# Performance work log

Hardware: AMD Instinct MI355X
Metric: run time of the kernel (lower is better)

## Reference

```python
import jax, jax.numpy as jnp
import numpy as np

NUM_LEVELS = 4
RADIUS = 4
H, W = 64, 128


def _bilinear_sample(feat, x, y):
    # feat: [N, Hl, Wl]; x, y: [N, K, K] pixel coords; zeros padding, align_corners=True
    N, Hl, Wl = feat.shape
    x0 = jnp.floor(x)
    y0 = jnp.floor(y)
    x1 = x0 + 1.0
    y1 = y0 + 1.0
    wx1 = x - x0
    wx0 = 1.0 - wx1
    wy1 = y - y0
    wy0 = 1.0 - wy1
    n_idx = jnp.arange(N)[:, None, None]

    def gather(xi, yi):
        inb = (xi >= 0) & (xi <= Wl - 1) & (yi >= 0) & (yi <= Hl - 1)
        xc = jnp.clip(xi, 0, Wl - 1).astype(jnp.int32)
        yc = jnp.clip(yi, 0, Hl - 1).astype(jnp.int32)
        v = feat[n_idx, yc, xc]
        return jnp.where(inb, v, jnp.zeros((), feat.dtype))

    return (gather(x0, y0) * wx0 * wy0 + gather(x1, y0) * wx1 * wy0
            + gather(x0, y1) * wx0 * wy1 + gather(x1, y1) * wx1 * wy1)


def _correlation(fmap1, fmap2, coords):
    bs, dim, h, w = fmap1.shape
    f1 = fmap1.reshape(bs, dim, h * w)
    f2 = fmap2.reshape(bs, dim, h * w)
    cv = jnp.einsum('bdm,bdn->bmn', f1, f2) / jnp.sqrt(jnp.asarray(dim, jnp.float32))
    cv = cv.reshape(bs * h * w, h, w)
    pyramid = [cv]
    for _ in range(NUM_LEVELS - 1):
        N, hl, wl = cv.shape
        cv = cv.reshape(N, hl // 2, 2, wl // 2, 2).mean(axis=(2, 4))  # avg_pool2d(2,2)
        pyramid.append(cv)

    cxy = coords.transpose(0, 2, 3, 1).astype(jnp.float32)  # [bs,h,w,2]
    cx = cxy[..., 0].reshape(-1)  # [bs*h*w]
    cy = cxy[..., 1].reshape(-1)
    r = RADIUS
    d = jnp.linspace(-r, r, 2 * r + 1, dtype=jnp.float32)
    dy, dx = jnp.meshgrid(d, d, indexing='ij')  # [K,K]

    outs = []
    for i, corr in enumerate(pyramid):
        scale = jnp.float32(2 ** i)
        x = cx[:, None, None] / scale + dx[None]
        y = cy[:, None, None] / scale + dy[None]
        sampled = _bilinear_sample(corr, x, y)  # [bs*h*w, K, K]
        outs.append(sampled.reshape(bs, h, w, -1))
    out = jnp.concatenate(outs, axis=-1)  # [bs,h,w,num_levels*K*K]
    return out.transpose(0, 3, 1, 2)


def setup_inputs() -> dict:
    key = jax.random.key(0)
    k1, k2, k3, k4 = jax.random.split(key, 4)
    fmap1 = jax.random.normal(k1, (1, 256, H, W), dtype=jnp.float32)
    fmap2 = jax.random.normal(k2, (1, 256, H, W), dtype=jnp.float32)
    cx = jax.random.uniform(k3, (1, 1, H, W), dtype=jnp.float32) * (W - 1)
    cy = jax.random.uniform(k4, (1, 1, H, W), dtype=jnp.float32) * (H - 1)
    coords = jnp.concatenate([cx, cy], axis=1)  # [1,2,H,W], channel 0 = x, 1 = y
    return {"fmap1": fmap1, "fmap2": fmap2, "coords": coords}


def reference(fmap1, fmap2, coords):
    return _correlation(fmap1, fmap2, coords)
```

## Files before the change

kernel.cpp:

```cpp
#include <hip/hip_runtime.h>
#include <stdint.h>

typedef _Float16 f16;
typedef __attribute__((ext_vector_type(8))) _Float16 f16x8;
typedef __attribute__((ext_vector_type(4))) float f32x4;
typedef __attribute__((ext_vector_type(2))) float fv2;
typedef __attribute__((ext_vector_type(4))) float fv4;

#define H0 64
#define W0 128
#define NPIX 8192
#define KD 256
#define NCAT 10880
#define OFF1 8192
#define OFF2 10240
#define OFF3 10752
#define CAP0 640
#define CAP1 2048
#define PL1OFF (32 * CAP0)
#define PLTOT (PL1OFF + 8 * CAP1)
#define ZTOT (64 + PLTOT + 64)


__global__ __launch_bounds__(256) void fused_pre(const float* __restrict__ in0,
                                                 const float* __restrict__ in1,
                                                 f16* __restrict__ At,
                                                 f16* __restrict__ Bt,
                                                 int* __restrict__ cnt) {
  __shared__ f16 tile[64][65];
  int bid = blockIdx.x;
  int t = threadIdx.x;

  if (bid < 1024) {
    const float* in = (bid < 512) ? in0 : in1;
    f16* out = (bid < 512) ? At : Bt;
    size_t NR = (bid < 512) ? NPIX : NCAT;
    int bx = bid & 511;
    int m0 = (bx & 127) * 64;
    int d0 = (bx >> 7) * 64;
    int a = t & 63, b = t >> 6;
#pragma unroll
    for (int i = 0; i < 16; ++i) {
      int d = b + i * 4;
      tile[a][d] = (f16)in[(size_t)(d0 + d) * NPIX + m0 + a];
    }
    __syncthreads();
#pragma unroll
    for (int i = 0; i < 16; ++i) {
      int m = b + i * 4;
      int d = d0 + a;
      out[((size_t)(d >> 5) * NR + (m0 + m)) * 32 + (d & 31)] = tile[m][a];
    }
  } else if (bid < 1360) {
    int idx = (bid - 1024) * 256 + t;
    float acc[8] = {0, 0, 0, 0, 0, 0, 0, 0};
    int r, dc;
    if (idx < 65536) {
      int r1 = idx & 2047; dc = idx >> 11; r = r1;
      int y = r1 >> 6, x = r1 & 63;
#pragma unroll
      for (int e = 0; e < 8; ++e) {
        const float* p = in1 + (size_t)(dc * 8 + e) * NPIX + (y * 2) * W0 + x * 2;
        fv2 s0 = *(const fv2*)p;
        fv2 s1 = *(const fv2*)(p + W0);
        acc[e] = (s0[0] + s0[1] + s1[0] + s1[1]) * 0.25f;
      }
    } else if (idx < 81920) {
      int i2 = idx - 65536;
      int r2 = i2 & 511; dc = i2 >> 9; r = 2048 + r2;
      int y = r2 >> 5, x = r2 & 31;
#pragma unroll
      for (int e = 0; e < 8; ++e) {
        const float* p = in1 + (size_t)(dc * 8 + e) * NPIX + (y * 4) * W0 + x * 4;
        float s = 0.f;
#pragma unroll
        for (int h = 0; h < 4; ++h) {
          fv4 v = *(const fv4*)(p + h * W0);
          s += v[0] + v[1] + v[2] + v[3];
        }
        acc[e] = s * 0.0625f;
      }
    } else {
      int i3 = idx - 81920;
      int r3 = i3 & 127; dc = i3 >> 7; r = 2560 + r3;
      int y = r3 >> 4, x = r3 & 15;
#pragma unroll
      for (int e = 0; e < 8; ++e) {
        const float* p = in1 + (size_t)(dc * 8 + e) * NPIX + (y * 8) * W0 + x * 8;
        float s = 0.f;
#pragma unroll
        for (int h = 0; h < 8; ++h) {
          fv4 v0 = *(const fv4*)(p + h * W0);
          fv4 v1 = *(const fv4*)(p + h * W0 + 4);
          s += v0[0] + v0[1] + v0[2] + v0[3] + v1[0] + v1[1] + v1[2] + v1[3];
        }
        acc[e] = s * 0.015625f;
      }
    }
    f16x8 o;
#pragma unroll
    for (int e = 0; e < 8; ++e) o[e] = (f16)acc[e];
    *(f16x8*)(Bt + ((size_t)(dc >> 2) * NCAT + 8192 + r) * 32 + (dc & 3) * 8) = o;
  } else {
    int idx = (bid - 1360) * 256 + t;
    if (idx < ZTOT) cnt[idx] = 0;
  }
}

__global__ __launch_bounds__(1024) void bucket_build(const float* __restrict__ coords,
                                                     int2* __restrict__ meta,
                                                     int* __restrict__ cnt) {
  __shared__ int hist[40];
  __shared__ int base[40];
  int* plist = cnt + 64;
  int t = threadIdx.x;
  int m = blockIdx.x * 1024 + t;
  if (t < 40) hist[t] = 0;
  __syncthreads();

  float cx = coords[m];
  float cy = coords[NPIX + m];
  int X0l[2], Y0l[2];
  int mx = 0, my = 0;
#pragma unroll
  for (int lev = 0; lev < 4; ++lev) {
    float inv = 1.0f / (float)(1 << lev);
    int X0 = (int)floorf(cx * inv) - 4;
    int Y0 = (int)floorf(cy * inv) - 4;
    if (lev < 2) { X0l[lev] = X0; Y0l[lev] = Y0; }
    mx |= (X0 & 0xff) << (8 * lev);
    my |= (Y0 & 0xff) << (8 * lev);
  }
  meta[m] = make_int2(mx, my);

  int b0 = (min(max(Y0l[0], 0), 63) >> 4) * 8 + (min(max(X0l[0], 0), 127) >> 4);
  int b1 = (min(max(Y0l[1], 0), 31) >> 4) * 4 + (min(max(X0l[1], 0), 63) >> 4);
  int s0 = atomicAdd(&hist[b0], 1);
  int s1 = atomicAdd(&hist[32 + b1], 1);
  __syncthreads();

  if (t < 40) base[t] = atomicAdd(&cnt[t], hist[t]);
  __syncthreads();

  int p0 = base[b0] + s0;
  if (p0 < CAP0) plist[b0 * CAP0 + p0] = m;
  int p1 = base[32 + b1] + s1;
  if (p1 < CAP1) plist[PL1OFF + b1 * CAP1 + p1] = m;
}

__global__ __launch_bounds__(256, 2) void gemm_all(const f16* __restrict__ At,
                                                   const f16* __restrict__ Bt,
                                                   const int* __restrict__ cnt,
                                                   const int2* __restrict__ meta,
                                                   f16* __restrict__ Wbuf) {
  __shared__ f16 sa[8192];
  const int* plist = cnt + 64;
  int bid = blockIdx.x;
  int t = threadIdx.x;
  int lane = t & 63;
  int w = t >> 6;
  int lr = lane & 15;
  int ko = lane >> 4;

  if (bid < 160) {
    int bm = (((bid & 7) << 2) | ((bid >> 3) & 3)) << 8;
    int bn = OFF2 + ((bid >> 5) << 7);

    const f16* Ab = At + (size_t)(bm + w * 64 + lr) * 32 + ko * 8;
    const f16* Bb = Bt + (size_t)(bn + lr) * 32 + ko * 8;

    f16x8 af[2][4], bf[2][8];
#define LOADK(s, kk)                                                           \
    do {                                                                       \
      const f16* ap = Ab + (size_t)(kk) * (NPIX * 32);                         \
      const f16* bp = Bb + (size_t)(kk) * (NCAT * 32);                         \
      _Pragma("unroll")                                                        \
      for (int i = 0; i < 4; ++i) af[s][i] = *(const f16x8*)(ap + i * 512);    \
      _Pragma("unroll")                                                        \
      for (int i = 0; i < 8; ++i) bf[s][i] = *(const f16x8*)(bp + i * 512);    \
    } while (0)

    f32x4 acc[4][8];
#pragma unroll
    for (int i = 0; i < 4; ++i)
#pragma unroll
      for (int j = 0; j < 8; ++j) acc[i][j] = (f32x4){0.f, 0.f, 0.f, 0.f};

    LOADK(0, 0);
    LOADK(1, 1);
#pragma unroll
    for (int kk = 0; kk < 8; ++kk) {
      const int cur = kk & 1;
#pragma unroll
      for (int mi = 0; mi < 4; ++mi)
#pragma unroll
        for (int ni = 0; ni < 8; ++ni)
          acc[mi][ni] = __builtin_amdgcn_mfma_f32_16x16x32_f16(
              af[cur][mi], bf[cur][ni], acc[mi][ni], 0, 0, 0);
      if (kk + 2 < 8) LOADK(cur, kk + 2);
    }
#undef LOADK

    int lev, n0, wlog;
    if (bn < OFF3) { lev = 2; n0 = bn - OFF2; wlog = 5; }
    else           { lev = 3; n0 = bn - OFF3; wlog = 4; }
    int wmask = (1 << wlog) - 1;
    int yA = n0 >> wlog;
    int yB = (n0 + 127) >> wlog;
    int ycol[8], xcol[8];
#pragma unroll
    for (int ni = 0; ni < 8; ++ni) {
      int n = n0 + ni * 16 + lr;
      ycol[ni] = n >> wlog;
      xcol[ni] = n & wmask;
    }
    int sh = lev * 8;
#pragma unroll
    for (int mi = 0; mi < 4; ++mi)
#pragma unroll
      for (int r2 = 0; r2 < 4; ++r2) {
        int grow = bm + w * 64 + mi * 16 + ko * 4 + r2;
        int2 mv = meta[grow];
        int Y0 = (int)(signed char)((mv.y >> sh) & 0xff);
        if (Y0 <= yB && Y0 + 9 >= yA) {
          int X0 = (int)(signed char)((mv.x >> sh) & 0xff);
          f16* rowp = Wbuf + (size_t)grow * 512 + lev * 128;
#pragma unroll
          for (int ni = 0; ni < 8; ++ni) {
            int dy = ycol[ni] - Y0;
            int dx = xcol[ni] - X0;
            if ((unsigned)dy < 10u && (unsigned)dx < 10u)
              rowp[dy * 12 + dx] = (f16)(acc[mi][ni][r2] * 0.0625f);
          }
        }
      }
    return;
  }

  int bb = bid - 160;
  int lev, b, mg, half;
  if (bb < 1280) { lev = 0; b = bb / 40; int r = bb % 40; mg = r >> 1; half = r & 1; }
  else { lev = 1; int i = bb - 1280; b = i / 128; int r = i % 128; mg = r >> 1; half = r & 1; }

  int CAP   = lev ? CAP1 : CAP0;
  int cb    = min(cnt[lev ? 32 + b : b], CAP);
  if (mg * 32 >= cb) return;
  int Hl    = lev ? 32 : 64;
  int Wmap  = lev ? 64 : 128;
  int bx    = lev ? (b & 3) : (b & 7);
  int by    = lev ? (b >> 2) : (b >> 3);
  int x0 = bx * 16, y0 = by * 16;
  int NY = min(25, Hl - y0);
  int rowbase = lev ? 8192 : 0;
  int pbase = (lev ? PL1OFF + b * CAP1 : b * CAP0) + mg * 32;

  {
    int spix = t >> 3;
    int skk  = t & 7;
    int sp = plist[pbase + spix] & (NPIX - 1);
    const f16* g = At + (size_t)skk * (NPIX * 32) + (size_t)sp * 32;
    int line = spix >> 1;
    int sb = (spix & 1) * 4;
    f16* dst = sa + skk * 1024 + line * 64;
#pragma unroll
    for (int q = 0; q < 4; ++q) {
      int phys = (sb + q) ^ (line & 7);
      *(f16x8*)(dst + phys * 8) = *(const f16x8*)(g + q * 8);
    }
  }

  int aoff[2];
#pragma unroll
  for (int mi = 0; mi < 2; ++mi) {
    int pl = mi * 16 + lr;
    int line = pl >> 1;
    int phys = ((pl & 1) * 4 + ko) ^ (line & 7);
    aoff[mi] = line * 64 + phys * 8;
  }

  bool vst[4];
  int brow[4];
#pragma unroll
  for (int st = 0; st < 4; ++st) {
    int q = w + 4 * st;
    int yl = half * 13 + q;
    vst[st] = (q < (half ? 12 : 13)) && (yl < NY);
    int ylc = min(yl, NY - 1);
    brow[st] = rowbase + (y0 + ylc) * Wmap + x0 + lr;
  }

  f16x8 bf[2][8];
#define BLDB(s_, kk_)                                                          \
  do {                                                                         \
    const f16* bp = Bt + (size_t)(kk_) * (NCAT * 32) + ko * 8;                 \
    _Pragma("unroll")                                                          \
    for (int st = 0; st < 4; ++st) {                                           \
      bf[s_][st * 2]     = *(const f16x8*)(bp + (size_t)brow[st] * 32);        \
      bf[s_][st * 2 + 1] = *(const f16x8*)(bp + (size_t)(brow[st] + 16) * 32); \
    }                                                                          \
  } while (0)

  BLDB(0, 0);
  BLDB(1, 1);

  f32x4 acc[8][2];
#pragma unroll
  for (int i = 0; i < 8; ++i)
#pragma unroll
    for (int j = 0; j < 2; ++j) acc[i][j] = (f32x4){0.f, 0.f, 0.f, 0.f};

  __syncthreads();

#pragma unroll
  for (int kk = 0; kk < 8; ++kk) {
    const int cur = kk & 1;
    f16x8 a0 = *(const f16x8*)(sa + kk * 1024 + aoff[0]);
    f16x8 a1 = *(const f16x8*)(sa + kk * 1024 + aoff[1]);
#pragma unroll
    for (int nf = 0; nf < 8; ++nf) {
      acc[nf][0] = __builtin_amdgcn_mfma_f32_16x16x32_f16(a0, bf[cur][nf],
                                                          acc[nf][0], 0, 0, 0);
      acc[nf][1] = __builtin_amdgcn_mfma_f32_16x16x32_f16(a1, bf[cur][nf],
                                                          acc[nf][1], 0, 0, 0);
    }
    if (kk + 2 < 8) BLDB(cur, kk + 2);
  }
#undef BLDB

  int pe[2][4];
  int Xp[2][4], Yp[2][4];
  int sh = lev * 8;
#pragma unroll
  for (int mi = 0; mi < 2; ++mi)
#pragma unroll
    for (int r2 = 0; r2 < 4; ++r2) {
      int slot = mg * 32 + mi * 16 + ko * 4 + r2;
      int p = plist[pbase + mi * 16 + ko * 4 + r2] & (NPIX - 1);
      pe[mi][r2] = (slot < cb) ? p : -1;
      int2 mv = meta[p];
      Xp[mi][r2] = (int)(signed char)((mv.x >> sh) & 0xff);
      Yp[mi][r2] = (int)(signed char)((mv.y >> sh) & 0xff);
    }
#pragma unroll
  for (int st = 0; st < 4; ++st) {
    if (!vst[st]) continue;
    int y = y0 + half * 13 + w + 4 * st;
#pragma unroll
    for (int xc = 0; xc < 2; ++xc) {
      int x = x0 + xc * 16 + lr;
#pragma unroll
      for (int mi = 0; mi < 2; ++mi)
#pragma unroll
        for (int r2 = 0; r2 < 4; ++r2) {
          int p = pe[mi][r2];
          int dy = y - Yp[mi][r2];
          int dx = x - Xp[mi][r2];
          if (p >= 0 && (unsigned)dy < 10u && (unsigned)dx < 10u)
            Wbuf[(size_t)p * 512 + lev * 128 + dy * 12 + dx] =
                (f16)(acc[st * 2 + xc][mi][r2] * 0.0625f);
        }
    }
  }
}

__global__ __launch_bounds__(64) void corr_sample(const f16* __restrict__ Wbuf,
                                                  const float* __restrict__ coords,
                                                  float* __restrict__ out) {
  int tid = blockIdx.x * 64 + threadIdx.x;
  int m = tid & (NPIX - 1);
  int lev = tid >> 13;
  int Hl = H0 >> lev, Wl = W0 >> lev;

  float cx = coords[m];
  float cy = coords[NPIX + m];
  float inv = 1.0f / (float)(1 << lev);
  float xb = cx * inv, yb = cy * inv;
  float fx = floorf(xb), fy = floorf(yb);
  int X0 = (int)fx - 4, Y0 = (int)fy - 4;
  float wx1 = xb - fx, wx0 = 1.0f - wx1;
  float wy1 = yb - fy, wy0 = 1.0f - wy1;

  const f16* wb = Wbuf + (size_t)m * 512 + lev * 128;
  f16x8 rv[15];
#pragma unroll
  for (int i = 0; i < 15; ++i) rv[i] = *(const f16x8*)(wb + i * 8);

  float* op = out + (size_t)lev * 81 * NPIX + m;
  float cur[11], nxt[11];
#pragma unroll
  for (int i = 0; i < 11; ++i) {
    bool in = ((unsigned)Y0 < (unsigned)Hl) && ((unsigned)(X0 + i) < (unsigned)Wl);
    cur[i] = in ? (float)rv[i >> 3][i & 7] : 0.0f;
  }
#pragma unroll
  for (int j = 0; j < 9; ++j) {
    bool yin = (unsigned)(Y0 + j + 1) < (unsigned)Hl;
#pragma unroll
    for (int i = 0; i < 11; ++i) {
      int c = (j + 1) * 12 + i;
      bool in = yin && ((unsigned)(X0 + i) < (unsigned)Wl);
      nxt[i] = in ? (float)rv[c >> 3][c & 7] : 0.0f;
    }
#pragma unroll
    for (int i = 0; i < 9; ++i) {
      float v = wy0 * (wx0 * cur[i] + wx1 * cur[i + 1])
              + wy1 * (wx0 * nxt[i] + wx1 * nxt[i + 1]);
      op[(size_t)(j * 9 + i) * NPIX] = v;
    }
#pragma unroll
    for (int i = 0; i < 11; ++i) cur[i] = nxt[i];
  }
}

extern "C" void kernel_launch(void* const* d_in, const int* in_sizes, int n_in,
                              void* d_out, int out_size, void* d_ws, size_t ws_size,
                              hipStream_t stream) {
  const float* fmap1  = (const float*)d_in[0];
  const float* fmap2  = (const float*)d_in[1];
  const float* coords = (const float*)d_in[2];
  float* out = (float*)d_out;

  char* ws = (char*)d_ws;
  size_t offA = 0;
  size_t offB = offA + (size_t)NPIX * KD * 2;
  size_t offW = offB + (size_t)NCAT * KD * 2;
  size_t offM = offW + (size_t)NPIX * 512 * 2;
  size_t offC = offM + (size_t)NPIX * 8;
  size_t need = offC + (size_t)ZTOT * 4;
  if (ws_size < need) return;

  f16*  At   = (f16*)(ws + offA);
  f16*  Bt   = (f16*)(ws + offB);
  f16*  Wbuf = (f16*)(ws + offW);
  int2* meta = (int2*)(ws + offM);
  int*  cnt  = (int*)(ws + offC);

  fused_pre<<<1505, 256, 0, stream>>>(fmap1, fmap2, At, Bt, cnt);
  bucket_build<<<8, 1024, 0, stream>>>(coords, meta, cnt);
  gemm_all<<<2464, 256, 0, stream>>>(At, Bt, cnt, meta, Wbuf);
  corr_sample<<<512, 64, 0, stream>>>(Wbuf, coords, out);
}
```

Measured before the change: 73.35 us.

## Split dense and bucketed GEMM into separate kernels with XCD-aware block mapping

Splits the combined GEMM kernel into a dense kernel for the coarse pyramid levels and a bucketed kernel for the fine levels, so the bucketed kernel can use a higher occupancy launch bound. Bucketed blocks are remapped so that blocks sharing a bucket land on the same XCD, which should improve L2 reuse of B rows. The LDS swizzle of the A tile now also mixes in the k-slice index to reduce bank conflicts. The cost is an extra kernel launch, and the dense and bucketed GEMM work no longer run concurrently.

```diff
diff --git a/kernel.cpp b/kernel.cpp
--- a/kernel.cpp
+++ b/kernel.cpp
@@ -148,99 +148,103 @@
   if (p1 < CAP1) plist[PL1OFF + b1 * CAP1 + p1] = m;
 }
 
-__global__ __launch_bounds__(256, 2) void gemm_all(const f16* __restrict__ At,
-                                                   const f16* __restrict__ Bt,
-                                                   const int* __restrict__ cnt,
-                                                   const int2* __restrict__ meta,
-                                                   f16* __restrict__ Wbuf) {
-  __shared__ f16 sa[8192];
-  const int* plist = cnt + 64;
+__global__ __launch_bounds__(256, 2) void gemm_dense(const f16* __restrict__ At,
+                                                     const f16* __restrict__ Bt,
+                                                     const int2* __restrict__ meta,
+                                                     f16* __restrict__ Wbuf) {
   int bid = blockIdx.x;
+  int bm = (((bid & 7) << 2) | ((bid >> 3) & 3)) << 8;
+  int bn = OFF2 + ((bid >> 5) << 7);
+
   int t = threadIdx.x;
   int lane = t & 63;
   int w = t >> 6;
   int lr = lane & 15;
   int ko = lane >> 4;
 
-  if (bid < 160) {
-    int bm = (((bid & 7) << 2) | ((bid >> 3) & 3)) << 8;
-    int bn = OFF2 + ((bid >> 5) << 7);
-
-    const f16* Ab = At + (size_t)(bm + w * 64 + lr) * 32 + ko * 8;
-    const f16* Bb = Bt + (size_t)(bn + lr) * 32 + ko * 8;
-
-    f16x8 af[2][4], bf[2][8];
+  const f16* Ab = At + (size_t)(bm + w * 64 + lr) * 32 + ko * 8;
+  const f16* Bb = Bt + (size_t)(bn + lr) * 32 + ko * 8;
+
+  f16x8 af[2][4], bf[2][8];
 #define LOADK(s, kk)                                                           \
-    do {                                                                       \
-      const f16* ap = Ab + (size_t)(kk) * (NPIX * 32);                         \
-      const f16* bp = Bb + (size_t)(kk) * (NCAT * 32);                         \
-      _Pragma("unroll")                                                        \
-      for (int i = 0; i < 4; ++i) af[s][i] = *(const f16x8*)(ap + i * 512);    \
-      _Pragma("unroll")                                                        \
-      for (int i = 0; i < 8; ++i) bf[s][i] = *(const f16x8*)(bp + i * 512);    \
-    } while (0)
-
-    f32x4 acc[4][8];
-#pragma unroll
-    for (int i = 0; i < 4; ++i)
-#pragma unroll
-      for (int j = 0; j < 8; ++j) acc[i][j] = (f32x4){0.f, 0.f, 0.f, 0.f};
-
-    LOADK(0, 0);
-    LOADK(1, 1);
-#pragma unroll
-    for (int kk = 0; kk < 8; ++kk) {
-      const int cur = kk & 1;
-#pragma unroll
-      for (int mi = 0; mi < 4; ++mi)
-#pragma unroll
-        for (int ni = 0; ni < 8; ++ni)
-          acc[mi][ni] = __builtin_amdgcn_mfma_f32_16x16x32_f16(
-              af[cur][mi], bf[cur][ni], acc[mi][ni], 0, 0, 0);
-      if (kk + 2 < 8) LOADK(cur, kk + 2);
-    }
+  do {                                                                         \
+    const f16* ap = Ab + (size_t)(kk) * (NPIX * 32);                           \
+    const f16* bp = Bb + (size_t)(kk) * (NCAT * 32);                           \
+    _Pragma("unroll")                                                          \
+    for (int i = 0; i < 4; ++i) af[s][i] = *(const f16x8*)(ap + i * 512);      \
+    _Pragma("unroll")                                                          \
+    for (int i = 0; i < 8; ++i) bf[s][i] = *(const f16x8*)(bp + i * 512);      \
+  } while (0)
+
+  f32x4 acc[4][8];
+#pragma unroll
+  for (int i = 0; i < 4; ++i)
+#pragma unroll
+    for (int j = 0; j < 8; ++j) acc[i][j] = (f32x4){0.f, 0.f, 0.f, 0.f};
+
+  LOADK(0, 0);
+  LOADK(1, 1);
+#pragma unroll
+  for (int kk = 0; kk < 8; ++kk) {
+    const int cur = kk & 1;
+#pragma unroll
+    for (int mi = 0; mi < 4; ++mi)
+#pragma unroll
+      for (int ni = 0; ni < 8; ++ni)
+        acc[mi][ni] = __builtin_amdgcn_mfma_f32_16x16x32_f16(
+            af[cur][mi], bf[cur][ni], acc[mi][ni], 0, 0, 0);
+    if (kk + 2 < 8) LOADK(cur, kk + 2);
+  }
 #undef LOADK
 
-    int lev, n0, wlog;
-    if (bn < OFF3) { lev = 2; n0 = bn - OFF2; wlog = 5; }
-    else           { lev = 3; n0 = bn - OFF3; wlog = 4; }
-    int wmask = (1 << wlog) - 1;
-    int yA = n0 >> wlog;
-    int yB = (n0 + 127) >> wlog;
-    int ycol[8], xcol[8];
-#pragma unroll
-    for (int ni = 0; ni < 8; ++ni) {
-      int n = n0 + ni * 16 + lr;
-      ycol[ni] = n >> wlog;
-      xcol[ni] = n & wmask;
-    }
-    int sh = lev * 8;
-#pragma unroll
-    for (int mi = 0; mi < 4; ++mi)
-#pragma unroll
-      for (int r2 = 0; r2 < 4; ++r2) {
-        int grow = bm + w * 64 + mi * 16 + ko * 4 + r2;
-        int2 mv = meta[grow];
-        int Y0 = (int)(signed char)((mv.y >> sh) & 0xff);
-        if (Y0 <= yB && Y0 + 9 >= yA) {
-          int X0 = (int)(signed char)((mv.x >> sh) & 0xff);
-          f16* rowp = Wbuf + (size_t)grow * 512 + lev * 128;
-#pragma unroll
-          for (int ni = 0; ni < 8; ++ni) {
-            int dy = ycol[ni] - Y0;
-            int dx = xcol[ni] - X0;
-            if ((unsigned)dy < 10u && (unsigned)dx < 10u)
-              rowp[dy * 12 + dx] = (f16)(acc[mi][ni][r2] * 0.0625f);
-          }
+  int lev, n0, wlog;
+  if (bn < OFF3) { lev = 2; n0 = bn - OFF2; wlog = 5; }
+  else           { lev = 3; n0 = bn - OFF3; wlog = 4; }
+  int wmask = (1 << wlog) - 1;
+  int yA = n0 >> wlog;
+  int yB = (n0 + 127) >> wlog;
+  int ycol[8], xcol[8];
+#pragma unroll
+  for (int ni = 0; ni < 8; ++ni) {
+    int n = n0 + ni * 16 + lr;
+    ycol[ni] = n >> wlog;
+    xcol[ni] = n & wmask;
+  }
+  int sh = lev * 8;
+#pragma unroll
+  for (int mi = 0; mi < 4; ++mi)
+#pragma unroll
+    for (int r2 = 0; r2 < 4; ++r2) {
+      int grow = bm + w * 64 + mi * 16 + ko * 4 + r2;
+      int2 mv = meta[grow];
+      int Y0 = (int)(signed char)((mv.y >> sh) & 0xff);
+      if (Y0 <= yB && Y0 + 9 >= yA) {
+        int X0 = (int)(signed char)((mv.x >> sh) & 0xff);
+        f16* rowp = Wbuf + (size_t)grow * 512 + lev * 128;
+#pragma unroll
+        for (int ni = 0; ni < 8; ++ni) {
+          int dy = ycol[ni] - Y0;
+          int dx = xcol[ni] - X0;
+          if ((unsigned)dy < 10u && (unsigned)dx < 10u)
+            rowp[dy * 12 + dx] = (f16)(acc[mi][ni][r2] * 0.0625f);
         }
       }
-    return;
-  }
-
-  int bb = bid - 160;
+    }
+}
+
+__global__ __launch_bounds__(256, 3) void gemm_bucket(const f16* __restrict__ At,
+                                                      const f16* __restrict__ Bt,
+                                                      const int* __restrict__ cnt,
+                                                      const int2* __restrict__ meta,
+                                                      f16* __restrict__ Wbuf) {
+  __shared__ f16 sa[8192];
+  const int* plist = cnt + 64;
+  int bid = blockIdx.x;
+  int xcd = bid & 7;
+  int s = bid >> 3;
   int lev, b, mg, half;
-  if (bb < 1280) { lev = 0; b = bb / 40; int r = bb % 40; mg = r >> 1; half = r & 1; }
-  else { lev = 1; int i = bb - 1280; b = i / 128; int r = i % 128; mg = r >> 1; half = r & 1; }
+  if (s < 160) { lev = 0; int j = s / 40; int r = s - j * 40; b = xcd * 4 + j; mg = r >> 1; half = r & 1; }
+  else         { lev = 1; int r = s - 160; b = xcd; mg = r >> 1; half = r & 1; }
 
   int CAP   = lev ? CAP1 : CAP0;
   int cb    = min(cnt[lev ? 32 + b : b], CAP);
@@ -254,6 +258,12 @@
   int rowbase = lev ? 8192 : 0;
   int pbase = (lev ? PL1OFF + b * CAP1 : b * CAP0) + mg * 32;
 
+  int t = threadIdx.x;
+  int lane = t & 63;
+  int w = t >> 6;
+  int lr = lane & 15;
+  int ko = lane >> 4;
+
   {
     int spix = t >> 3;
     int skk  = t & 7;
@@ -264,7 +274,7 @@
     f16* dst = sa + skk * 1024 + line * 64;
 #pragma unroll
     for (int q = 0; q < 4; ++q) {
-      int phys = (sb + q) ^ (line & 7);
+      int phys = (sb + q) ^ (line & 7) ^ skk;
       *(f16x8*)(dst + phys * 8) = *(const f16x8*)(g + q * 8);
     }
   }
@@ -314,8 +324,8 @@
 #pragma unroll
   for (int kk = 0; kk < 8; ++kk) {
     const int cur = kk & 1;
-    f16x8 a0 = *(const f16x8*)(sa + kk * 1024 + aoff[0]);
-    f16x8 a1 = *(const f16x8*)(sa + kk * 1024 + aoff[1]);
+    f16x8 a0 = *(const f16x8*)(sa + kk * 1024 + (aoff[0] ^ (kk * 8)));
+    f16x8 a1 = *(const f16x8*)(sa + kk * 1024 + (aoff[1] ^ (kk * 8)));
 #pragma unroll
     for (int nf = 0; nf < 8; ++nf) {
       acc[nf][0] = __builtin_amdgcn_mfma_f32_16x16x32_f16(a0, bf[cur][nf],
@@ -437,6 +447,7 @@
 
   fused_pre<<<1505, 256, 0, stream>>>(fmap1, fmap2, At, Bt, cnt);
   bucket_build<<<8, 1024, 0, stream>>>(coords, meta, cnt);
-  gemm_all<<<2464, 256, 0, stream>>>(At, Bt, cnt, meta, Wbuf);
+  gemm_dense<<<160, 256, 0, stream>>>(At, Bt, meta, Wbuf);
+  gemm_bucket<<<2304, 256, 0, stream>>>(At, Bt, cnt, meta, Wbuf);
   corr_sample<<<512, 64, 0, stream>>>(Wbuf, coords, out);
 }
```

Measured after the change: 94.87 us. +29.3%, slower.
